# Performance work log

Hardware: AMD Instinct MI355X
Metric: run time of the kernel (lower is better)

## Reference

```python
import jax, jax.numpy as jnp
import numpy as np

B, S, D, H = 4, 2048, 1024, 16
DK = D // H


def setup_inputs() -> dict:
    key = jax.random.key(0)
    ks = jax.random.split(key, 12)
    s = 1.0 / np.sqrt(D)
    return {
        "query": jax.random.normal(ks[0], (B, S, D), jnp.float32),
        "key": jax.random.normal(ks[1], (B, S, D), jnp.float32),
        "value": jax.random.normal(ks[2], (B, S, D), jnp.float32),
        "mask": jax.random.randint(ks[3], (B, S), 0, 2, jnp.int32),
        "wq": jax.random.normal(ks[4], (D, D), jnp.float32) * s,
        "bq": jnp.zeros((D,), jnp.float32),
        "wk": jax.random.normal(ks[5], (D, D), jnp.float32) * s,
        "bk": jnp.zeros((D,), jnp.float32),
        "wv": jax.random.normal(ks[6], (D, D), jnp.float32) * s,
        "bv": jnp.zeros((D,), jnp.float32),
        "wo": jax.random.normal(ks[7], (D, D), jnp.float32) * s,
        "bo": jnp.zeros((D,), jnp.float32),
    }


def reference(query, key, value, mask, wq, bq, wk, bk, wv, bv, wo, bo):
    # torch Linear: y = x @ W.T + b
    def proj(x, w, b):
        y = jnp.einsum('bsd,ed->bse', x, w) + b
        return y.reshape(B, S, H, DK).transpose(0, 2, 1, 3)  # [B,H,S,DK]

    q = proj(query, wq, bq)
    k = proj(key, wk, bk)
    v = proj(value, wv, bv)

    scores = jnp.einsum('bhqd,bhkd->bhqk', q, k) / jnp.sqrt(jnp.float32(DK))
    m = mask[:, None, None, :]  # [B,1,1,S_kv]
    scores = jnp.where(m == 0, jnp.float32(-1e9), scores)
    attn = jax.nn.softmax(scores, axis=-1)  # dropout p=0.0 (eval)
    out = jnp.einsum('bhqk,bhkd->bhqd', attn, v)
    out = out.transpose(0, 2, 1, 3).reshape(B, S, D)
    return jnp.einsum('bsd,ed->bse', out, wo) + bo
```

## Files before the change

### kernel.cpp

```cpp
#include <hip/hip_runtime.h>
#include <hip/hip_bf16.h>

typedef __bf16 bf16;
typedef bf16 bf16x2 __attribute__((ext_vector_type(2)));
typedef bf16 bf16x4 __attribute__((ext_vector_type(4)));
typedef bf16 bf16x8 __attribute__((ext_vector_type(8)));
typedef float f32x4 __attribute__((ext_vector_type(4)));
typedef float f32x16 __attribute__((ext_vector_type(16)));
typedef unsigned int u32;
typedef u32 u32x4 __attribute__((ext_vector_type(4)));

#define MFMA16(A,B,C) __builtin_amdgcn_mfma_f32_16x16x32_bf16(A,B,C,0,0,0)
#define MFMA32(A,B,C) __builtin_amdgcn_mfma_f32_32x32x16_bf16(A,B,C,0,0,0)

__device__ __forceinline__ void gld_lds16(const void* g, void* l) {
  __builtin_amdgcn_global_load_lds(
      (const __attribute__((address_space(1))) void*)g,
      (__attribute__((address_space(3))) void*)l, 16, 0, 0);
}

__device__ __forceinline__ float max3f(float a, float b, float c) {
  return fmaxf(fmaxf(a, b), c);
}

__global__ void cast3_kernel(const float* __restrict__ s0, const float* __restrict__ s1,
                             const float* __restrict__ s2,
                             bf16* __restrict__ d0, bf16* __restrict__ d1, bf16* __restrict__ d2) {
  const int which = blockIdx.x >> 13;
  const int i = (blockIdx.x & 8191) * 256 + threadIdx.x;
  const float* s = which == 0 ? s0 : which == 1 ? s1 : s2;
  bf16* d = which == 0 ? d0 : which == 1 ? d1 : d2;
  float4 v = ((const float4*)s)[i];
  bf16x4 o;
  o[0] = (bf16)v.x; o[1] = (bf16)v.y; o[2] = (bf16)v.z; o[3] = (bf16)v.w;
  *(bf16x4*)(d + (size_t)i * 4) = o;
}

__global__ void cast4_kernel(const float* __restrict__ s0, const float* __restrict__ s1,
                             const float* __restrict__ s2, const float* __restrict__ s3,
                             bf16* __restrict__ d0, bf16* __restrict__ d1,
                             bf16* __restrict__ d2, bf16* __restrict__ d3) {
  const int which = blockIdx.x >> 10;
  const int i = (blockIdx.x & 1023) * 256 + threadIdx.x;
  const float* s = which == 0 ? s0 : which == 1 ? s1 : which == 2 ? s2 : s3;
  bf16* d = which == 0 ? d0 : which == 1 ? d1 : which == 2 ? d2 : d3;
  float4 v = ((const float4*)s)[i];
  bf16x4 o;
  o[0] = (bf16)v.x; o[1] = (bf16)v.y; o[2] = (bf16)v.z; o[3] = (bf16)v.w;
  *(bf16x4*)(d + (size_t)i * 4) = o;
}

__global__ void maskf_kernel(const int* __restrict__ m, float* __restrict__ mf) {
  const int i = blockIdx.x * 256 + threadIdx.x;
  const int4 v = ((const int4*)m)[i];
  float4 o;
  o.x = v.x ? 0.0f : -1e9f;
  o.y = v.y ? 0.0f : -1e9f;
  o.z = v.z ? 0.0f : -1e9f;
  o.w = v.w ? 0.0f : -1e9f;
  ((float4*)mf)[i] = o;
}

__device__ __forceinline__ void gemm128_core(
    const bf16* __restrict__ aBase, const bf16* __restrict__ bBase,
    bf16* sA, bf16* sB, f32x4 (&acc)[4][4])
{
  const int t = threadIdx.x;
  const int lane = t & 63, w = t >> 6;
  const int c = lane & 15, g = lane >> 4;

  int srow[2], scol[2];
#pragma unroll
  for (int i = 0; i < 2; ++i) {
    const int P = i * 4096 + t * 16;
    const int L = P ^ (((P >> 7) & 7) << 4);
    srow[i] = L >> 6;
    scol[i] = (L & 63) >> 1;
  }

  auto stage = [&](int buf, int kt) {
#pragma unroll
    for (int i = 0; i < 2; ++i)
      gld_lds16(aBase + (size_t)srow[i] * 1024 + kt * 32 + scol[i],
                &sA[buf * 4096 + i * 2048 + t * 8]);
#pragma unroll
    for (int i = 0; i < 2; ++i)
      gld_lds16(bBase + (size_t)srow[i] * 1024 + kt * 32 + scol[i],
                &sB[buf * 4096 + i * 2048 + t * 8]);
  };

  auto rd = [&](const bf16* s, int row) -> bf16x8 {
    const int phys = (row * 64 + g * 16) ^ (((row >> 1) & 7) << 4);
    return *(const bf16x8*)((const char*)s + phys);
  };

  const int wr = w >> 1, wc = w & 1;

  stage(0, 0);
  int buf = 0;
#pragma unroll 1
  for (int kt = 0; kt < 32; ++kt) {
    __builtin_amdgcn_s_barrier();
    if (kt < 31) {
      stage(buf ^ 1, kt + 1);
      asm volatile("s_waitcnt vmcnt(4)" ::: "memory");
    } else {
      asm volatile("s_waitcnt vmcnt(0)" ::: "memory");
    }
    __builtin_amdgcn_s_barrier();

    const bf16* tA = sA + buf * 4096;
    const bf16* tB = sB + buf * 4096;
    bf16x8 af[4], bfr[4];
#pragma unroll
    for (int mi = 0; mi < 4; ++mi) af[mi] = rd(tA, wr * 64 + mi * 16 + c);
#pragma unroll
    for (int ni = 0; ni < 4; ++ni) bfr[ni] = rd(tB, wc * 64 + ni * 16 + c);
    __builtin_amdgcn_s_setprio(1);
#pragma unroll
    for (int mi = 0; mi < 4; ++mi)
#pragma unroll
      for (int ni = 0; ni < 4; ++ni)
        acc[mi][ni] = MFMA16(af[mi], bfr[ni], acc[mi][ni]);
    __builtin_amdgcn_s_setprio(0);
    buf ^= 1;
  }
}

__global__ __launch_bounds__(256) void qkv_gemm128(
    const bf16* __restrict__ qx, const bf16* __restrict__ kx, const bf16* __restrict__ vx,
    const bf16* __restrict__ wqb, const bf16* __restrict__ wkb, const bf16* __restrict__ wvb,
    const float* __restrict__ bq, const float* __restrict__ bk, const float* __restrict__ bv,
    bf16* __restrict__ qp, bf16* __restrict__ kp, bf16* __restrict__ vt, float qscale)
{
  __shared__ bf16 sA[2 * 4096];
  __shared__ bf16 sB[2 * 4096];
  const int z = blockIdx.z;
  const bf16* A    = z == 0 ? qx  : z == 1 ? kx  : vx;
  const bf16* Bm   = z == 0 ? wqb : z == 1 ? wkb : wvb;
  const float* bias = z == 0 ? bq : z == 1 ? bk : bv;
  const int bm = blockIdx.y, bn = blockIdx.x;

  f32x4 acc[4][4] = {};
  gemm128_core(A + (size_t)(bm * 128) * 1024, Bm + (size_t)(bn * 128) * 1024, sA, sB, acc);

  const int t = threadIdx.x, lane = t & 63, w = t >> 6;
  const int wr = w >> 1, wc = w & 1, c = lane & 15, g = lane >> 4;
  const float sc = z == 0 ? qscale : 1.0f;
  bf16* Cb = z == 0 ? qp : kp;
#pragma unroll
  for (int ni = 0; ni < 4; ++ni) {
    const int col = bn * 128 + wc * 64 + ni * 16 + c;
    const float bvv = bias[col];
#pragma unroll
    for (int mi = 0; mi < 4; ++mi) {
#pragma unroll
      for (int r4 = 0; r4 < 4; ++r4) {
        const int row = bm * 128 + wr * 64 + mi * 16 + g * 4 + r4;
        const float val = (acc[mi][ni][r4] + bvv) * sc;
        if (z == 2) {
          const int bb = row >> 11, s = row & 2047;
          vt[((size_t)(bb * 1024 + col)) * 2048 + s] = (bf16)val;
        } else {
          Cb[(size_t)row * 1024 + col] = (bf16)val;
        }
      }
    }
  }
}

__global__ __launch_bounds__(256) void out_gemm128(
    const bf16* __restrict__ A, const bf16* __restrict__ Bm,
    const float* __restrict__ bias, float* __restrict__ Cout)
{
  __shared__ bf16 sA[2 * 4096];
  __shared__ bf16 sB[2 * 4096];
  const int bm = blockIdx.y, bn = blockIdx.x;

  f32x4 acc[4][4] = {};
  gemm128_core(A + (size_t)(bm * 128) * 1024, Bm + (size_t)(bn * 128) * 1024, sA, sB, acc);

  const int t = threadIdx.x, lane = t & 63, w = t >> 6;
  const int wr = w >> 1, wc = w & 1, c = lane & 15, g = lane >> 4;
#pragma unroll
  for (int ni = 0; ni < 4; ++ni) {
    const int col = bn * 128 + wc * 64 + ni * 16 + c;
    const float bvv = bias[col];
#pragma unroll
    for (int mi = 0; mi < 4; ++mi) {
#pragma unroll
      for (int r4 = 0; r4 < 4; ++r4) {
        const int row = bm * 128 + wr * 64 + mi * 16 + g * 4 + r4;
        Cout[(size_t)row * 1024 + col] = acc[mi][ni][r4] + bvv;
      }
    }
  }
}

__global__ __launch_bounds__(256) void attn_kernel(
    const bf16* __restrict__ Qp, const bf16* __restrict__ Kp, const bf16* __restrict__ Vt,
    const float* __restrict__ maskf, bf16* __restrict__ Out)
{
  __shared__ bf16 sKV[2][64 * 128];

  const int bh = blockIdx.x;
  const int b = bh >> 4, h = bh & 15;
  const int t = threadIdx.x, lane = t & 63, w = t >> 6;
  const int q32 = lane & 31, hi = lane >> 5;
  const int q0 = blockIdx.y * 128 + w * 32;

  const char* kBase = (const char*)(Kp + (size_t)(b * 2048) * 1024 + h * 64);
  const char* vBase = (const char*)(Vt + (size_t)(bh * 64) * 2048);

  auto stageKV = [&](int buf, int kt) {
#pragma unroll
    for (int j = 0; j < 4; ++j) {
      const int P = j * 4096 + t * 16;
      const int L = P ^ (((P >> 8) & 15) << 4);
      const int row = L >> 8;
      const int off = L & 255;
      const char* src = (off < 128)
          ? kBase + (size_t)(kt * 64 + row) * 2048 + off
          : vBase + (size_t)row * 4096 + kt * 128 + (off - 128);
      gld_lds16(src, (char*)sKV[buf] + P);
    }
  };

  bf16x8 qf[4];
  const bf16* qrow = Qp + (size_t)(b * 2048 + q0 + q32) * 1024 + h * 64;
#pragma unroll
  for (int ks = 0; ks < 4; ++ks)
    qf[ks] = *(const bf16x8*)&qrow[ks * 16 + hi * 8];

  float mrun = -1e30f, lrun = 0.f;
  f32x16 aco[2] = {};

  const float* mrow = maskf + b * 2048;

  stageKV(0, 0);
  __syncthreads();
  int cur = 0;
  for (int kt = 0; kt < 32; ++kt) {
    if (kt + 1 < 32) stageKV(cur ^ 1, kt + 1);

    f32x16 st[2];
#pragma unroll
    for (int kf = 0; kf < 2; ++kf)
#pragma unroll
      for (int q4 = 0; q4 < 4; ++q4) {
        const float4 mm = *(const float4*)&mrow[kt * 64 + kf * 32 + q4 * 8 + hi * 4];
        st[kf][q4 * 4 + 0] = mm.x;
        st[kf][q4 * 4 + 1] = mm.y;
        st[kf][q4 * 4 + 2] = mm.z;
        st[kf][q4 * 4 + 3] = mm.w;
      }

#pragma unroll
    for (int ks = 0; ks < 4; ++ks) {
      bf16x8 k0f, k1f;
      {
        const int row = q32;
        const int phys = row * 256 + ((ks * 32 + hi * 16) ^ ((row & 15) << 4));
        k0f = *(const bf16x8*)((const char*)sKV[cur] + phys);
      }
      {
        const int row = 32 + q32;
        const int phys = row * 256 + ((ks * 32 + hi * 16) ^ ((row & 15) << 4));
        k1f = *(const bf16x8*)((const char*)sKV[cur] + phys);
      }
      __builtin_amdgcn_s_setprio(1);
      st[0] = MFMA32(k0f, qf[ks], st[0]);
      st[1] = MFMA32(k1f, qf[ks], st[1]);
      __builtin_amdgcn_s_setprio(0);
    }

    float c0 = max3f(st[0][0], st[0][1], st[0][2]);
    c0 = max3f(c0, st[0][3], st[0][4]);
    c0 = max3f(c0, st[0][5], st[0][6]);
    c0 = fmaxf(c0, st[0][7]);
    float c1 = max3f(st[0][8], st[0][9], st[0][10]);
    c1 = max3f(c1, st[0][11], st[0][12]);
    c1 = max3f(c1, st[0][13], st[0][14]);
    c1 = fmaxf(c1, st[0][15]);
    float c2 = max3f(st[1][0], st[1][1], st[1][2]);
    c2 = max3f(c2, st[1][3], st[1][4]);
    c2 = max3f(c2, st[1][5], st[1][6]);
    c2 = fmaxf(c2, st[1][7]);
    float c3 = max3f(st[1][8], st[1][9], st[1][10]);
    c3 = max3f(c3, st[1][11], st[1][12]);
    c3 = max3f(c3, st[1][13], st[1][14]);
    c3 = fmaxf(c3, st[1][15]);
    float tmax = fmaxf(max3f(c0, c1, c2), c3);
    tmax = fmaxf(tmax, __shfl_xor(tmax, 32, 64));
    if (!__all(tmax <= mrun + 11.5f)) {
      const float mnew = fmaxf(mrun, tmax);
      const float sc = exp2f(mrun - mnew);
      mrun = mnew;
      lrun *= sc;
      aco[0] *= sc;
      aco[1] *= sc;
    }
    float rs0 = 0.f, rs1 = 0.f, rs2 = 0.f, rs3 = 0.f;
#pragma unroll
    for (int i = 0; i < 16; i += 4) {
      float p00 = exp2f(st[0][i] - mrun),     p01 = exp2f(st[0][i + 1] - mrun);
      float p02 = exp2f(st[0][i + 2] - mrun), p03 = exp2f(st[0][i + 3] - mrun);
      float p10 = exp2f(st[1][i] - mrun),     p11 = exp2f(st[1][i + 1] - mrun);
      float p12 = exp2f(st[1][i + 2] - mrun), p13 = exp2f(st[1][i + 3] - mrun);
      st[0][i] = p00; st[0][i + 1] = p01; st[0][i + 2] = p02; st[0][i + 3] = p03;
      st[1][i] = p10; st[1][i + 1] = p11; st[1][i + 2] = p12; st[1][i + 3] = p13;
      rs0 += p00 + p01; rs1 += p02 + p03;
      rs2 += p10 + p11; rs3 += p12 + p13;
    }
    float rs = (rs0 + rs1) + (rs2 + rs3);
    rs += __shfl_xor(rs, 32, 64);
    lrun += rs;

    bf16x8 pa[4];
#pragma unroll
    for (int kf = 0; kf < 2; ++kf) {
      u32 u[4][2];
#pragma unroll
      for (int g2 = 0; g2 < 4; ++g2) {
        asm("v_cvt_pk_bf16_f32 %0, %1, %2"
            : "=v"(u[g2][0]) : "v"(st[kf][4 * g2 + 0]), "v"(st[kf][4 * g2 + 1]));
        asm("v_cvt_pk_bf16_f32 %0, %1, %2"
            : "=v"(u[g2][1]) : "v"(st[kf][4 * g2 + 2]), "v"(st[kf][4 * g2 + 3]));
      }
      u32 d0 = u[0][0], d2 = u[1][0];
      asm("v_permlane32_swap_b32 %0, %1" : "+v"(d0), "+v"(d2));
      u32 d1 = u[0][1], d3 = u[1][1];
      asm("v_permlane32_swap_b32 %0, %1" : "+v"(d1), "+v"(d3));
      u32x4 ud = {d0, d1, d2, d3};
      pa[2 * kf] = __builtin_bit_cast(bf16x8, ud);
      u32 e0 = u[2][0], e2 = u[3][0];
      asm("v_permlane32_swap_b32 %0, %1" : "+v"(e0), "+v"(e2));
      u32 e1 = u[2][1], e3 = u[3][1];
      asm("v_permlane32_swap_b32 %0, %1" : "+v"(e1), "+v"(e3));
      u32x4 ue = {e0, e1, e2, e3};
      pa[2 * kf + 1] = __builtin_bit_cast(bf16x8, ue);
    }

#pragma unroll
    for (int kk = 0; kk < 4; ++kk) {
      bf16x8 vb0, vb1;
      {
        const int row = q32;
        const int phys = row * 256 + ((128 + kk * 32 + hi * 16) ^ ((row & 15) << 4));
        vb0 = *(const bf16x8*)((const char*)sKV[cur] + phys);
      }
      {
        const int row = 32 + q32;
        const int phys = row * 256 + ((128 + kk * 32 + hi * 16) ^ ((row & 15) << 4));
        vb1 = *(const bf16x8*)((const char*)sKV[cur] + phys);
      }
      __builtin_amdgcn_s_setprio(1);
      aco[0] = MFMA32(vb0, pa[kk], aco[0]);
      aco[1] = MFMA32(vb1, pa[kk], aco[1]);
      __builtin_amdgcn_s_setprio(0);
    }

    __syncthreads();
    cur ^= 1;
  }

  const float inv = 1.0f / lrun;
  bf16* orow = Out + (size_t)(b * 2048 + q0 + q32) * 1024 + h * 64;
#pragma unroll
  for (int dkf = 0; dkf < 2; ++dkf)
#pragma unroll
    for (int q4 = 0; q4 < 4; ++q4) {
      bf16x4 o;
#pragma unroll
      for (int r4 = 0; r4 < 4; ++r4)
        o[r4] = (bf16)(aco[dkf][q4 * 4 + r4] * inv);
      *(bf16x4*)&orow[dkf * 32 + q4 * 8 + hi * 4] = o;
    }
}

extern "C" void kernel_launch(void* const* d_in, const int* in_sizes, int n_in,
                              void* d_out, int out_size, void* d_ws, size_t ws_size,
                              hipStream_t stream) {
  const float* q  = (const float*)d_in[0];
  const float* k  = (const float*)d_in[1];
  const float* v  = (const float*)d_in[2];
  const int*  msk = (const int*)d_in[3];
  const float* wq = (const float*)d_in[4];
  const float* bq = (const float*)d_in[5];
  const float* wk = (const float*)d_in[6];
  const float* bk = (const float*)d_in[7];
  const float* wv = (const float*)d_in[8];
  const float* bv = (const float*)d_in[9];
  const float* wo = (const float*)d_in[10];
  const float* bo = (const float*)d_in[11];

  bf16* ws = (bf16*)d_ws;
  const size_t NEL = 8192ull * 1024ull;
  bf16* qx  = ws;
  bf16* kx  = ws + NEL;
  bf16* vx  = ws + 2 * NEL;
  bf16* wqb = ws + 3 * NEL;
  bf16* wkb = wqb + 1048576;
  bf16* wvb = wkb + 1048576;
  bf16* wob = wvb + 1048576;
  bf16* qp  = wob + 1048576;
  bf16* kp  = qp + NEL;
  bf16* vt  = kp + NEL;
  float* mf = (float*)(vt + NEL);
  bf16* ao  = vx;

  cast3_kernel<<<24576, 256, 0, stream>>>(q, k, v, qx, kx, vx);
  cast4_kernel<<<4096, 256, 0, stream>>>(wq, wk, wv, wo, wqb, wkb, wvb, wob);
  maskf_kernel<<<8, 256, 0, stream>>>(msk, mf);

  const float qscale = 0.125f * 1.44269504088896f;
  qkv_gemm128<<<dim3(8, 64, 3), 256, 0, stream>>>(qx, kx, vx, wqb, wkb, wvb,
                                                  bq, bk, bv, qp, kp, vt, qscale);
  attn_kernel<<<dim3(64, 16), 256, 0, stream>>>(qp, kp, vt, mf, ao);
  out_gemm128<<<dim3(8, 64), 256, 0, stream>>>(ao, wob, bo, (float*)d_out);
}
```

Before: 435.3 us.

## Enlarge GEMM tiles to 256x256 with 8 waves and triple-buffered LDS pipeline

Both projection GEMMs move from 128x128 tiles with 4 waves and double buffering to 256x256 tiles with 8 waves and a three-slot LDS ring. Loads are issued two k-steps ahead and split into A and B halves placed between MFMA phases. The goal is more operand reuse per global byte and better hiding of load latency. The attention kernel also precomputes K/V source pointers and advances them by stride instead of recomputing addresses each tile. The trade-off is fewer blocks (384 and 128), which leaves the out-projection with fewer blocks than the MI355X has CUs, plus more registers and LDS per block.

```diff
diff --git a/kernel.cpp b/kernel.cpp
--- a/kernel.cpp
+++ b/kernel.cpp
@@ -61,61 +61,59 @@
   ((float4*)mf)[i] = o;
 }
 
-__device__ __forceinline__ void gemm128_core(
+__device__ __forceinline__ void gemm256_core(
     const bf16* __restrict__ aBase, const bf16* __restrict__ bBase,
-    bf16* sA, bf16* sB, f32x4 (&acc)[4][4])
+    bf16* sA, bf16* sB, f32x4 (&acc)[8][4])
 {
   const int t = threadIdx.x;
   const int lane = t & 63, w = t >> 6;
+  const int wm = w >> 2, wn = w & 3;
   const int c = lane & 15, g = lane >> 4;
 
-  int srow[2], scol[2];
-#pragma unroll
-  for (int i = 0; i < 2; ++i) {
-    const int P = i * 4096 + t * 16;
-    const int L = P ^ (((P >> 7) & 7) << 4);
-    srow[i] = L >> 6;
-    scol[i] = (L & 63) >> 1;
-  }
-
-  auto stage = [&](int buf, int kt) {
-#pragma unroll
-    for (int i = 0; i < 2; ++i)
-      gld_lds16(aBase + (size_t)srow[i] * 1024 + kt * 32 + scol[i],
-                &sA[buf * 4096 + i * 2048 + t * 8]);
-#pragma unroll
-    for (int i = 0; i < 2; ++i)
-      gld_lds16(bBase + (size_t)srow[i] * 1024 + kt * 32 + scol[i],
-                &sB[buf * 4096 + i * 2048 + t * 8]);
+  const int P = t * 16;
+  const int L = P ^ (((P >> 7) & 7) << 4);
+  const int srow = L >> 6;
+  const int scol = (L & 63) >> 1;
+
+  auto stageA = [&](int slot, int kt) {
+#pragma unroll
+    for (int r = 0; r < 2; ++r)
+      gld_lds16(aBase + (size_t)(r * 128 + srow) * 1024 + kt * 32 + scol,
+                &sA[slot * 8192 + r * 4096 + t * 8]);
   };
-
+  auto stageB = [&](int slot, int kt) {
+#pragma unroll
+    for (int r = 0; r < 2; ++r)
+      gld_lds16(bBase + (size_t)(r * 128 + srow) * 1024 + kt * 32 + scol,
+                &sB[slot * 8192 + r * 4096 + t * 8]);
+  };
   auto rd = [&](const bf16* s, int row) -> bf16x8 {
     const int phys = (row * 64 + g * 16) ^ (((row >> 1) & 7) << 4);
     return *(const bf16x8*)((const char*)s + phys);
   };
 
-  const int wr = w >> 1, wc = w & 1;
-
-  stage(0, 0);
-  int buf = 0;
+  stageA(0, 0); stageB(0, 0);
+  stageA(1, 1); stageB(1, 1);
+
+  int slot = 0;
 #pragma unroll 1
   for (int kt = 0; kt < 32; ++kt) {
+    int s2 = slot + 2; if (s2 >= 3) s2 -= 3;
+    if (kt < 31) asm volatile("s_waitcnt vmcnt(4)" ::: "memory");
+    else         asm volatile("s_waitcnt vmcnt(0)" ::: "memory");
     __builtin_amdgcn_s_barrier();
-    if (kt < 31) {
-      stage(buf ^ 1, kt + 1);
-      asm volatile("s_waitcnt vmcnt(4)" ::: "memory");
-    } else {
-      asm volatile("s_waitcnt vmcnt(0)" ::: "memory");
-    }
-    __builtin_amdgcn_s_barrier();
-
-    const bf16* tA = sA + buf * 4096;
-    const bf16* tB = sB + buf * 4096;
-    bf16x8 af[4], bfr[4];
-#pragma unroll
-    for (int mi = 0; mi < 4; ++mi) af[mi] = rd(tA, wr * 64 + mi * 16 + c);
-#pragma unroll
-    for (int ni = 0; ni < 4; ++ni) bfr[ni] = rd(tB, wc * 64 + ni * 16 + c);
+    asm volatile("" ::: "memory");
+
+    const bf16* tA = sA + slot * 8192;
+    const bf16* tB = sB + slot * 8192;
+
+    bf16x8 bfr[4], af[4];
+#pragma unroll
+    for (int ni = 0; ni < 4; ++ni) bfr[ni] = rd(tB, wn * 64 + ni * 16 + c);
+#pragma unroll
+    for (int mi = 0; mi < 4; ++mi) af[mi] = rd(tA, wm * 128 + mi * 16 + c);
+    if (kt < 30) stageA(s2, kt + 2);
+    asm volatile("s_waitcnt lgkmcnt(0)" ::: "memory");
     __builtin_amdgcn_s_setprio(1);
 #pragma unroll
     for (int mi = 0; mi < 4; ++mi)
@@ -123,40 +121,54 @@
       for (int ni = 0; ni < 4; ++ni)
         acc[mi][ni] = MFMA16(af[mi], bfr[ni], acc[mi][ni]);
     __builtin_amdgcn_s_setprio(0);
-    buf ^= 1;
+    __builtin_amdgcn_s_barrier();
+
+#pragma unroll
+    for (int mi = 0; mi < 4; ++mi) af[mi] = rd(tA, wm * 128 + (mi + 4) * 16 + c);
+    if (kt < 30) stageB(s2, kt + 2);
+    asm volatile("s_waitcnt lgkmcnt(0)" ::: "memory");
+    __builtin_amdgcn_s_setprio(1);
+#pragma unroll
+    for (int mi = 0; mi < 4; ++mi)
+#pragma unroll
+      for (int ni = 0; ni < 4; ++ni)
+        acc[mi + 4][ni] = MFMA16(af[mi], bfr[ni], acc[mi + 4][ni]);
+    __builtin_amdgcn_s_setprio(0);
+
+    slot += 1; if (slot >= 3) slot = 0;
   }
 }
 
-__global__ __launch_bounds__(256) void qkv_gemm128(
+__global__ __launch_bounds__(512, 2) void qkv_gemm256(
     const bf16* __restrict__ qx, const bf16* __restrict__ kx, const bf16* __restrict__ vx,
     const bf16* __restrict__ wqb, const bf16* __restrict__ wkb, const bf16* __restrict__ wvb,
     const float* __restrict__ bq, const float* __restrict__ bk, const float* __restrict__ bv,
     bf16* __restrict__ qp, bf16* __restrict__ kp, bf16* __restrict__ vt, float qscale)
 {
-  __shared__ bf16 sA[2 * 4096];
-  __shared__ bf16 sB[2 * 4096];
+  __shared__ bf16 sA[3 * 8192];
+  __shared__ bf16 sB[3 * 8192];
   const int z = blockIdx.z;
   const bf16* A    = z == 0 ? qx  : z == 1 ? kx  : vx;
   const bf16* Bm   = z == 0 ? wqb : z == 1 ? wkb : wvb;
   const float* bias = z == 0 ? bq : z == 1 ? bk : bv;
   const int bm = blockIdx.y, bn = blockIdx.x;
 
-  f32x4 acc[4][4] = {};
-  gemm128_core(A + (size_t)(bm * 128) * 1024, Bm + (size_t)(bn * 128) * 1024, sA, sB, acc);
+  f32x4 acc[8][4] = {};
+  gemm256_core(A + (size_t)(bm * 256) * 1024, Bm + (size_t)(bn * 256) * 1024, sA, sB, acc);
 
   const int t = threadIdx.x, lane = t & 63, w = t >> 6;
-  const int wr = w >> 1, wc = w & 1, c = lane & 15, g = lane >> 4;
+  const int wm = w >> 2, wn = w & 3, c = lane & 15, g = lane >> 4;
   const float sc = z == 0 ? qscale : 1.0f;
   bf16* Cb = z == 0 ? qp : kp;
 #pragma unroll
   for (int ni = 0; ni < 4; ++ni) {
-    const int col = bn * 128 + wc * 64 + ni * 16 + c;
+    const int col = bn * 256 + wn * 64 + ni * 16 + c;
     const float bvv = bias[col];
 #pragma unroll
-    for (int mi = 0; mi < 4; ++mi) {
+    for (int mi = 0; mi < 8; ++mi) {
 #pragma unroll
       for (int r4 = 0; r4 < 4; ++r4) {
-        const int row = bm * 128 + wr * 64 + mi * 16 + g * 4 + r4;
+        const int row = bm * 256 + wm * 128 + mi * 16 + g * 4 + r4;
         const float val = (acc[mi][ni][r4] + bvv) * sc;
         if (z == 2) {
           const int bb = row >> 11, s = row & 2047;
@@ -169,28 +181,28 @@
   }
 }
 
-__global__ __launch_bounds__(256) void out_gemm128(
+__global__ __launch_bounds__(512, 2) void out_gemm256(
     const bf16* __restrict__ A, const bf16* __restrict__ Bm,
     const float* __restrict__ bias, float* __restrict__ Cout)
 {
-  __shared__ bf16 sA[2 * 4096];
-  __shared__ bf16 sB[2 * 4096];
+  __shared__ bf16 sA[3 * 8192];
+  __shared__ bf16 sB[3 * 8192];
   const int bm = blockIdx.y, bn = blockIdx.x;
 
-  f32x4 acc[4][4] = {};
-  gemm128_core(A + (size_t)(bm * 128) * 1024, Bm + (size_t)(bn * 128) * 1024, sA, sB, acc);
+  f32x4 acc[8][4] = {};
+  gemm256_core(A + (size_t)(bm * 256) * 1024, Bm + (size_t)(bn * 256) * 1024, sA, sB, acc);
 
   const int t = threadIdx.x, lane = t & 63, w = t >> 6;
-  const int wr = w >> 1, wc = w & 1, c = lane & 15, g = lane >> 4;
+  const int wm = w >> 2, wn = w & 3, c = lane & 15, g = lane >> 4;
 #pragma unroll
   for (int ni = 0; ni < 4; ++ni) {
-    const int col = bn * 128 + wc * 64 + ni * 16 + c;
+    const int col = bn * 256 + wn * 64 + ni * 16 + c;
     const float bvv = bias[col];
 #pragma unroll
-    for (int mi = 0; mi < 4; ++mi) {
+    for (int mi = 0; mi < 8; ++mi) {
 #pragma unroll
       for (int r4 = 0; r4 < 4; ++r4) {
-        const int row = bm * 128 + wr * 64 + mi * 16 + g * 4 + r4;
+        const int row = bm * 256 + wm * 128 + mi * 16 + g * 4 + r4;
         Cout[(size_t)row * 1024 + col] = acc[mi][ni][r4] + bvv;
       }
     }
@@ -212,18 +224,25 @@
   const char* kBase = (const char*)(Kp + (size_t)(b * 2048) * 1024 + h * 64);
   const char* vBase = (const char*)(Vt + (size_t)(bh * 64) * 2048);
 
-  auto stageKV = [&](int buf, int kt) {
-#pragma unroll
-    for (int j = 0; j < 4; ++j) {
-      const int P = j * 4096 + t * 16;
-      const int L = P ^ (((P >> 8) & 15) << 4);
-      const int row = L >> 8;
-      const int off = L & 255;
-      const char* src = (off < 128)
-          ? kBase + (size_t)(kt * 64 + row) * 2048 + off
-          : vBase + (size_t)row * 4096 + kt * 128 + (off - 128);
-      gld_lds16(src, (char*)sKV[buf] + P);
-    }
+  const char* srcp[4];
+  int strd[4];
+#pragma unroll
+  for (int j = 0; j < 4; ++j) {
+    const int P = j * 4096 + t * 16;
+    const int L = P ^ (((P >> 8) & 15) << 4);
+    const int row = L >> 8;
+    const int off = L & 255;
+    if (off < 128) { srcp[j] = kBase + (size_t)row * 2048 + off;         strd[j] = 131072; }
+    else           { srcp[j] = vBase + (size_t)row * 4096 + (off - 128); strd[j] = 128; }
+  }
+  auto stageKV = [&](int buf) {
+#pragma unroll
+    for (int j = 0; j < 4; ++j)
+      gld_lds16(srcp[j], (char*)sKV[buf] + j * 4096 + t * 16);
+  };
+  auto advKV = [&]() {
+#pragma unroll
+    for (int j = 0; j < 4; ++j) srcp[j] += strd[j];
   };
 
   bf16x8 qf[4];
@@ -237,11 +256,12 @@
 
   const float* mrow = maskf + b * 2048;
 
-  stageKV(0, 0);
+  stageKV(0);
+  advKV();
   __syncthreads();
   int cur = 0;
   for (int kt = 0; kt < 32; ++kt) {
-    if (kt + 1 < 32) stageKV(cur ^ 1, kt + 1);
+    if (kt + 1 < 32) { stageKV(cur ^ 1); advKV(); }
 
     f32x16 st[2];
 #pragma unroll
@@ -414,8 +434,8 @@
   maskf_kernel<<<8, 256, 0, stream>>>(msk, mf);
 
   const float qscale = 0.125f * 1.44269504088896f;
-  qkv_gemm128<<<dim3(8, 64, 3), 256, 0, stream>>>(qx, kx, vx, wqb, wkb, wvb,
+  qkv_gemm256<<<dim3(4, 32, 3), 512, 0, stream>>>(qx, kx, vx, wqb, wkb, wvb,
                                                   bq, bk, bv, qp, kp, vt, qscale);
   attn_kernel<<<dim3(64, 16), 256, 0, stream>>>(qp, kp, vt, mf, ao);
-  out_gemm128<<<dim3(8, 64), 256, 0, stream>>>(ao, wob, bo, (float*)d_out);
-}
+  out_gemm256<<<dim3(4, 32), 512, 0, stream>>>(ao, wob, bo, (float*)d_out);
+}
```

Result: slower. 450.5 us (+3.5%).
